# Optimization experiments

Measured on AMD Instinct MI355X. Metric: run time of the kernel, lower is better.

## Reference

```python
import jax, jax.numpy as jnp
import numpy as np
from jax import lax

HEADS = 6      # n_splits // head_ratio
DHEAD = 64     # hidden // n_splits
ALLH = HEADS * DHEAD  # 384
KS = 9         # conv_kernel_size
PAD = (KS - 1) // 2


def setup_inputs() -> dict:
    key = jax.random.key(0)
    ks = jax.random.split(key, 12)
    B, S, H = 8, 1024, 768
    f = jnp.float32
    return {
        "Q": jax.random.normal(ks[0], (B, S, H), f),
        "K": jax.random.normal(ks[1], (B, S, H), f),
        "V": jax.random.normal(ks[2], (B, S, H), f),
        "Wq": jax.random.normal(ks[3], (H, ALLH), f) * 0.02,
        "Wk": jax.random.normal(ks[4], (H, ALLH), f) * 0.02,
        "Wv": jax.random.normal(ks[5], (H, ALLH), f) * 0.02,
        "dw": jax.random.normal(ks[6], (H, KS), f) * 0.02,        # depthwise conv [C,k]
        "pw": jax.random.normal(ks[7], (ALLH, H), f) * 0.02,      # pointwise conv [out,in]
        "sep_bias": jnp.zeros((ALLH,), f),
        "Wck": jax.random.normal(ks[8], (ALLH, HEADS * KS), f) * 0.02,
        "bck": jnp.zeros((HEADS * KS,), f),
        "Wco": jax.random.normal(ks[9], (H, ALLH), f) * 0.02,
        "bco": jnp.zeros((ALLH,), f),
        "gammas": jnp.zeros((HEADS, 1, 1), f),
        "mask": jnp.ones((B, S), jnp.int32),
    }


def _forward(Q, K, V, Wq, Wk, Wv, dw, pw, sep_bias, Wck, bck, Wco, bco, gammas, mask):
    B, S, H = Q.shape
    q = Q @ Wq  # [B,S,ALLH]
    k = K @ Wk
    v = V @ Wv
    # SeparableConv1D on K: depthwise 'same' conv (groups=H) then 1x1 pointwise + bias
    x = K.transpose(0, 2, 1)  # [B,H,S]
    x = lax.conv_general_dilated(x, dw[:, None, :], (1,), [(PAD, PAD)],
                                 dimension_numbers=("NCH", "OIH", "NCH"),
                                 feature_group_count=H)
    keyconv = jnp.einsum("bcs,oc->bso", x, pw) + sep_bias  # [B,S,ALLH]
    # span-dynamic-conv kernel weights, softmax over kernel taps
    conv_attn = keyconv * q
    kern = (conv_attn @ Wck + bck).reshape(B, S, HEADS, KS)
    kern = jax.nn.softmax(kern, axis=-1)
    # unfold V-projection into local windows and apply per-position kernels
    co = V @ Wco + bco                                   # [B,S,ALLH]
    cop = jnp.pad(co, ((0, 0), (PAD, PAD), (0, 0)))
    win = jnp.stack([cop[:, j:j + S, :] for j in range(KS)], axis=-1)  # [B,S,ALLH,KS]
    win = win.reshape(B, S, HEADS, DHEAD, KS)
    conv_out = jnp.einsum("bshdk,bshk->bshd", win, kern)  # [B,S,HEADS,DHEAD]
    # standard attention scores
    q4 = q.reshape(B, S, HEADS, DHEAD).transpose(0, 2, 1, 3)
    k4 = k.reshape(B, S, HEADS, DHEAD).transpose(0, 2, 1, 3)
    v4 = v.reshape(B, S, HEADS, DHEAD).transpose(0, 2, 1, 3)
    scores = jnp.einsum("bhid,bhjd->bhij", q4, k4) / jnp.sqrt(jnp.float32(DHEAD))
    m = (mask != 0)[:, None, None, :]  # key mask [B,1,1,S]
    # monotonic distance scores (no-grad in original -> stop_gradient)
    sc = lax.stop_gradient(scores)
    p_ = jax.nn.softmax(jnp.where(m, sc, -1e32), axis=-1) * m.astype(sc.dtype)
    cum = jnp.cumsum(p_, axis=-1)
    tot = jnp.sum(p_, axis=-1, keepdims=True)
    idx = jnp.arange(S)
    pos = jnp.abs(idx[None, :] - idx[:, None]).astype(jnp.float32)  # |i-j|
    dist = jnp.sqrt(jnp.clip((tot - cum) * pos, 0.0))
    gamma = -jax.nn.softplus(gammas)[None]  # [1,HEADS,1,1]
    effect = jnp.clip(jnp.exp(dist * gamma), 1e-5, 1e5)
    scores2 = jnp.where(m, scores * effect, -1e8)
    probs = jax.nn.softmax(scores2, axis=-1)  # dropout_p=0 -> identity
    ctx = jnp.einsum("bhij,bhjd->bihd", probs, v4)  # [B,S,HEADS,DHEAD]
    out = jnp.concatenate([ctx, conv_out], axis=2).reshape(B, S, 2 * ALLH)
    return out


def reference(Q, K, V, Wq, Wk, Wv, dw, pw, sep_bias, Wck, bck, Wco, bco, gammas, mask):
    return _forward(Q, K, V, Wq, Wk, Wv, dw, pw, sep_bias, Wck, bck, Wco, bco, gammas, mask)
```

## Files before the change

kernel.cpp:

```cpp
#include <hip/hip_runtime.h>
#include <math.h>

#define BATCH 8
#define SEQ   1024
#define HID   768
#define HEADS 6
#define DHEAD 64
#define ALLH  384
#define KS    9
#define PADC  4
#define MROWS (BATCH*SEQ)

typedef __attribute__((ext_vector_type(8))) short bf16x8;
typedef __attribute__((ext_vector_type(4))) short bf16x4;
typedef __attribute__((ext_vector_type(4))) float f32x4;

__device__ __forceinline__ ushort f2bf(float x) {
    unsigned u = __float_as_uint(x);
    unsigned r = (u + 0x7FFFu + ((u >> 16) & 1u)) >> 16;
    return (ushort)r;
}
__device__ __forceinline__ unsigned pk2(float a, float b) {
    return (unsigned)f2bf(a) | ((unsigned)f2bf(b) << 16);
}
__device__ __forceinline__ float fexp2(float x) {
#if __has_builtin(__builtin_amdgcn_exp2f)
    return __builtin_amdgcn_exp2f(x);
#else
    return exp2f(x);
#endif
}
__device__ __forceinline__ float fsqrt(float x) {
#if __has_builtin(__builtin_amdgcn_sqrtf)
    return __builtin_amdgcn_sqrtf(x);
#else
    return __sqrtf(x);
#endif
}
__device__ __forceinline__ unsigned cvtpk(float a, float b) {
    unsigned r; asm("v_cvt_pk_bf16_f32 %0, %1, %2" : "=v"(r) : "v"(a), "v"(b)); return r;
}

__device__ __forceinline__ void mfma16(f32x4& c4, bf16x4 a, bf16x4 b) {
#if __has_builtin(__builtin_amdgcn_mfma_f32_16x16x16bf16_1k)
    c4 = __builtin_amdgcn_mfma_f32_16x16x16bf16_1k(a, b, c4, 0, 0, 0);
#else
    asm volatile("v_mfma_f32_16x16x16_bf16 %0, %1, %2, %0" : "+v"(c4) : "v"(a), "v"(b));
#endif
}

__global__ __launch_bounds__(256) void dconv_kernel(const float* __restrict__ Kin,
                                                    const float* __restrict__ dw,
                                                    ushort* __restrict__ y) {
    const int t = threadIdx.x;
    const int c4l = t & 63;
    const int sg = t >> 6;
    const int c4 = blockIdx.x * 64 + c4l;
    const int s0 = blockIdx.y * 64 + sg * 16;
    const int b = blockIdx.z;
    const int c = c4 * 4;

    const float* base = Kin + (size_t)b * SEQ * HID + c;
    ushort* ybase = y + (size_t)b * SEQ * HID + c;

    float wv[4][KS];
#pragma unroll
    for (int j = 0; j < 4; ++j)
#pragma unroll
        for (int tt = 0; tt < KS; ++tt) wv[j][tt] = dw[(c + j) * KS + tt];

    float4 win[KS];
#pragma unroll
    for (int tt = 0; tt < KS; ++tt) {
        int sj = s0 - PADC + tt;
        win[tt] = (sj >= 0 && sj < SEQ) ? *reinterpret_cast<const float4*>(base + (size_t)sj * HID)
                                        : float4{0.f, 0.f, 0.f, 0.f};
    }

#pragma unroll
    for (int i = 0; i < 16; ++i) {
        const int s = s0 + i;
        float4 acc = {0.f, 0.f, 0.f, 0.f};
#pragma unroll
        for (int tt = 0; tt < KS; ++tt) {
            acc.x += win[tt].x * wv[0][tt];
            acc.y += win[tt].y * wv[1][tt];
            acc.z += win[tt].z * wv[2][tt];
            acc.w += win[tt].w * wv[3][tt];
        }
        uint2 o;
        o.x = pk2(acc.x, acc.y); o.y = pk2(acc.z, acc.w);
        *reinterpret_cast<uint2*>(ybase + (size_t)s * HID) = o;
#pragma unroll
        for (int tt = 0; tt < KS - 1; ++tt) win[tt] = win[tt + 1];
        int sj = s + 1 + PADC;
        win[KS - 1] = (sj < SEQ) ? *reinterpret_cast<const float4*>(base + (size_t)sj * HID)
                                 : float4{0.f, 0.f, 0.f, 0.f};
    }
}

__global__ __launch_bounds__(256) void wcvt_kernel(const float* __restrict__ W0, const float* __restrict__ W1,
                                                   const float* __restrict__ W2, const float* __restrict__ W3,
                                                   ushort* __restrict__ O0, ushort* __restrict__ O1,
                                                   ushort* __restrict__ O2, ushort* __restrict__ O3) {
    __shared__ float t[32][33];
    int wsel = blockIdx.z;
    const float* W = wsel == 0 ? W0 : wsel == 1 ? W1 : wsel == 2 ? W2 : W3;
    ushort* O = wsel == 0 ? O0 : wsel == 1 ? O1 : wsel == 2 ? O2 : O3;
    int kt = blockIdx.x * 32;
    int nt = blockIdx.y * 32;
    int tx = threadIdx.x & 31, ty = threadIdx.x >> 5;
#pragma unroll
    for (int i = 0; i < 4; ++i)
        t[ty + i * 8][tx] = W[(size_t)(kt + ty + i * 8) * ALLH + nt + tx];
    __syncthreads();
#pragma unroll
    for (int i = 0; i < 4; ++i)
        O[(size_t)(nt + ty + i * 8) * HID + kt + tx] = f2bf(t[tx][ty + i * 8]);
}

__global__ __launch_bounds__(256) void pwcvt_kernel(const float* __restrict__ pw, ushort* __restrict__ pwb) {
    int i = blockIdx.x * 256 + threadIdx.x;
    if (i < ALLH * HID) pwb[i] = f2bf(pw[i]);
}

__global__ __launch_bounds__(256) void gemm_all(const float* __restrict__ Q,
                                                const float* __restrict__ Kin,
                                                const float* __restrict__ V,
                                                const ushort* __restrict__ ybf,
                                                const ushort* __restrict__ WqT,
                                                const ushort* __restrict__ WkT,
                                                const ushort* __restrict__ WvT,
                                                const ushort* __restrict__ WcoT,
                                                const ushort* __restrict__ pwT,
                                                const float* __restrict__ bco,
                                                const float* __restrict__ sep_bias,
                                                float* __restrict__ qb,
                                                ushort* __restrict__ qh,
                                                ushort* __restrict__ khm,
                                                ushort* __restrict__ vhm,
                                                float* __restrict__ cob,
                                                float* __restrict__ kcb) {
    __shared__ __align__(16) ushort As[64 * 64];
    __shared__ __align__(16) ushort Bs[64 * 64];

    const int bx = blockIdx.x;
    const int swz = (bx & 7) * 480 + (bx >> 3);
    const int unit = swz / 768;
    const int local = swz % 768;
    const int n0 = (local % 6) * 64;
    const int m0 = (local / 6) * 64;

    const float* Af = unit == 0 ? Q : unit == 1 ? Kin : V;
    const ushort* Ab = ybf;
    const ushort* Bt = unit == 0 ? WqT : unit == 1 ? WkT : unit == 2 ? WvT : unit == 3 ? WcoT : pwT;
    const bool af32 = (unit != 4);

    const int tid = threadIdx.x;
    const int lane = tid & 63;
    const int w = tid >> 6;
    const int g = lane >> 4;
    const int c = lane & 15;

    const int r0 = tid >> 3;
    const int r1 = r0 + 32;
    const int c8 = (tid & 7) * 8;
    const int b0 = r0 * 128 + ((c8 * 2) ^ ((r0 & 7) << 4));
    const int b1 = r1 * 128 + ((c8 * 2) ^ ((r1 & 7) << 4));

    uint4 ar0, ar1, br0, br1;
    float4 f0a, f0b, f1a, f1b;
    auto loadAB = [&](int k0) {
        if (af32) {
            f0a = *reinterpret_cast<const float4*>(&Af[(size_t)(m0 + r0) * HID + k0 + c8]);
            f0b = *reinterpret_cast<const float4*>(&Af[(size_t)(m0 + r0) * HID + k0 + c8 + 4]);
            f1a = *reinterpret_cast<const float4*>(&Af[(size_t)(m0 + r1) * HID + k0 + c8]);
            f1b = *reinterpret_cast<const float4*>(&Af[(size_t)(m0 + r1) * HID + k0 + c8 + 4]);
        } else {
            ar0 = *reinterpret_cast<const uint4*>(&Ab[(size_t)(m0 + r0) * HID + k0 + c8]);
            ar1 = *reinterpret_cast<const uint4*>(&Ab[(size_t)(m0 + r1) * HID + k0 + c8]);
        }
        br0 = *reinterpret_cast<const uint4*>(&Bt[(size_t)(n0 + r0) * HID + k0 + c8]);
        br1 = *reinterpret_cast<const uint4*>(&Bt[(size_t)(n0 + r1) * HID + k0 + c8]);
    };
    loadAB(0);

    f32x4 acc[4] = {{0,0,0,0},{0,0,0,0},{0,0,0,0},{0,0,0,0}};

    const int arow = w * 16 + c;
    const int asw = (arow & 7) << 4;

    for (int ks = 0; ks < 12; ++ks) {
        __syncthreads();
        if (af32) {
            uint4 p0, p1;
            p0.x = pk2(f0a.x, f0a.y); p0.y = pk2(f0a.z, f0a.w);
            p0.z = pk2(f0b.x, f0b.y); p0.w = pk2(f0b.z, f0b.w);
            p1.x = pk2(f1a.x, f1a.y); p1.y = pk2(f1a.z, f1a.w);
            p1.z = pk2(f1b.x, f1b.y); p1.w = pk2(f1b.z, f1b.w);
            *reinterpret_cast<uint4*>((char*)As + b0) = p0;
            *reinterpret_cast<uint4*>((char*)As + b1) = p1;
        } else {
            *reinterpret_cast<uint4*>((char*)As + b0) = ar0;
            *reinterpret_cast<uint4*>((char*)As + b1) = ar1;
        }
        *reinterpret_cast<uint4*>((char*)Bs + b0) = br0;
        *reinterpret_cast<uint4*>((char*)Bs + b1) = br1;
        __syncthreads();
        if (ks < 11) loadAB((ks + 1) * 64);

        bf16x8 af0 = *reinterpret_cast<const bf16x8*>((char*)As + arow * 128 + ((g * 16) ^ asw));
        bf16x8 af1 = *reinterpret_cast<const bf16x8*>((char*)As + arow * 128 + ((64 + g * 16) ^ asw));
#pragma unroll
        for (int nq = 0; nq < 4; ++nq) {
            const int brow = nq * 16 + c;
            const int bsw = (brow & 7) << 4;
            bf16x8 bf0 = *reinterpret_cast<const bf16x8*>((char*)Bs + brow * 128 + ((g * 16) ^ bsw));
            bf16x8 bf1 = *reinterpret_cast<const bf16x8*>((char*)Bs + brow * 128 + ((64 + g * 16) ^ bsw));
            acc[nq] = __builtin_amdgcn_mfma_f32_16x16x32_bf16(af0, bf0, acc[nq], 0, 0, 0);
            acc[nq] = __builtin_amdgcn_mfma_f32_16x16x32_bf16(af1, bf1, acc[nq], 0, 0, 0);
        }
    }

    if (unit == 2) {
        const int head = n0 >> 6;
        const int bb = m0 >> 10;
        const int st = (m0 & 1023) >> 6;
        char* tb = (char*)vhm + (((size_t)(bb * HEADS + head) * 16 + st) * 4096) * 2;
#pragma unroll
        for (int nq = 0; nq < 4; ++nq) {
            const int d = nq * 16 + c;
            unsigned off = (unsigned)d * 128 + (((unsigned)(32 * w + 8 * g)) ^ ((d & 7) << 4));
            uint2 vv;
            vv.x = pk2(acc[nq][0], acc[nq][1]);
            vv.y = pk2(acc[nq][2], acc[nq][3]);
            *reinterpret_cast<uint2*>(tb + off) = vv;
        }
        return;
    }

#pragma unroll
    for (int nq = 0; nq < 4; ++nq) {
        const int n = n0 + nq * 16 + c;
        float bv = 0.f;
        if (unit == 3) bv = bco[n];
        if (unit == 4) bv = sep_bias[n];
#pragma unroll
        for (int r = 0; r < 4; ++r) {
            const int m = m0 + w * 16 + g * 4 + r;
            float v = acc[nq][r] + bv;
            if (unit == 0) {
                qb[(size_t)m * ALLH + n] = v;
                int bb = m >> 10, s = m & 1023;
                int head = n >> 6, d = n & 63;
                qh[(((size_t)bb * HEADS + head) * SEQ + s) * 64 + d] = f2bf(v);
            } else if (unit == 1) {
                int bb = m >> 10, s = m & 1023;
                int head = n >> 6, d = n & 63;
                char* tb = (char*)khm + (((size_t)(bb * HEADS + head) * 16 + (s >> 6)) * 4096) * 2;
                unsigned off = (unsigned)(s & 63) * 128 + (((unsigned)(d * 2)) ^ ((s & 7) << 4));
                *reinterpret_cast<ushort*>(tb + off) = f2bf(v);
            } else if (unit == 3) {
                cob[(size_t)m * ALLH + n] = v;
            } else {
                kcb[(size_t)m * ALLH + n] = v;
            }
        }
    }
}

__global__ __launch_bounds__(256) void spankern_kernel(const float* __restrict__ keyconv,
                                                       const float* __restrict__ q,
                                                       const float* __restrict__ Wck,
                                                       const float* __restrict__ bck,
                                                       float* __restrict__ kern_sm) {
    __shared__ float ca[4][ALLH];
    __shared__ float kv[4][64];
    int row0 = blockIdx.x * 4;
    int tid = threadIdx.x;
    int r = tid >> 6;
    int lane = tid & 63;
    int row = row0 + r;
    for (int e = lane; e < ALLH; e += 64) {
        size_t off = (size_t)row * ALLH + e;
        ca[r][e] = keyconv[off] * q[off];
    }
    __syncthreads();
    float val = 0.f;
    if (lane < HEADS * KS) {
        for (int kidx = 0; kidx < ALLH; ++kidx)
            val += ca[r][kidx] * Wck[kidx * (HEADS * KS) + lane];
        val += bck[lane];
    }
    kv[r][lane] = val;
    __syncthreads();
    if (lane < HEADS) {
        float mx = -INFINITY;
#pragma unroll
        for (int t = 0; t < KS; ++t) mx = fmaxf(mx, kv[r][lane * KS + t]);
        float e[KS];
        float sum = 0.f;
#pragma unroll
        for (int t = 0; t < KS; ++t) {
            e[t] = expf(kv[r][lane * KS + t] - mx);
            sum += e[t];
        }
        float inv = 1.f / sum;
#pragma unroll
        for (int t = 0; t < KS; ++t)
            kern_sm[((size_t)row * HEADS + lane) * KS + t] = e[t] * inv;
    }
}

__global__ __launch_bounds__(256) void convout_kernel(const float* __restrict__ co,
                                                      const float* __restrict__ kern_sm,
                                                      float* __restrict__ out) {
    int idx = blockIdx.x * 256 + threadIdx.x;
    if (idx >= MROWS * (ALLH / 4)) return;
    int c4 = idx % (ALLH / 4);
    int s = (idx / (ALLH / 4)) % SEQ;
    int b = idx / ((ALLH / 4) * SEQ);
    int c = c4 * 4;
    int h = c >> 6;
    const float* ks = &kern_sm[(((size_t)b * SEQ + s) * HEADS + h) * KS];
    float kt[KS];
#pragma unroll
    for (int t = 0; t < KS; ++t) kt[t] = ks[t];
    float4 acc = {0.f, 0.f, 0.f, 0.f};
#pragma unroll
    for (int t = 0; t < KS; ++t) {
        int sj = s + t - PADC;
        if (sj >= 0 && sj < SEQ) {
            const float4 cv = *reinterpret_cast<const float4*>(&co[((size_t)b * SEQ + sj) * ALLH + c]);
            acc.x += cv.x * kt[t];
            acc.y += cv.y * kt[t];
            acc.z += cv.z * kt[t];
            acc.w += cv.w * kt[t];
        }
    }
    *reinterpret_cast<float4*>(&out[((size_t)b * SEQ + s) * (2 * ALLH) + ALLH + c]) = acc;
}

__global__ __launch_bounds__(256) void attn_mfma(const ushort* __restrict__ qh,
                                                 const ushort* __restrict__ kh,
                                                 const ushort* __restrict__ vh,
                                                 const int* __restrict__ mask,
                                                 const float* __restrict__ gammas,
                                                 float* __restrict__ out) {
    __shared__ __align__(16) ushort kbuf[64 * 64];
    __shared__ __align__(16) ushort vbuf[64 * 64];
    __shared__ float s_msk[SEQ];

    const int bid = blockIdx.x;
    const int blk = (bid & 7) * 96 + (bid >> 3);
    const int qt = blk & 15;
    const int h = (blk >> 4) % HEADS;
    const int b = blk / (16 * HEADS);
    const int i0 = qt * 64;
    const int tid = threadIdx.x;
    const int lane = tid & 63;
    const int w = tid >> 6;
    const int g = lane >> 4;
    const int c = lane & 15;

    const float LOG2E = 1.44269504f;
    float g0 = gammas[h];
    float gamma2 = -(fmaxf(g0, 0.f) + log1pf(expf(-fabsf(g0)))) * LOG2E;
    const float SLOG2 = 0.125f * LOG2E;

    const ushort* ktiles = kh + ((size_t)(b * HEADS + h) * 16) * 4096;
    const ushort* vtiles = vh + ((size_t)(b * HEADS + h) * 16) * 4096;
    const ushort* qhb = qh + ((size_t)b * HEADS + h) * SEQ * 64;

    for (int e = tid; e < SEQ; e += 256)
        s_msk[e] = (mask[b * SEQ + e] != 0) ? 1.f : 0.f;

    bf16x8 qf0, qf1;
    {
        const ushort* qrow = qhb + (size_t)(i0 + w * 16 + c) * 64 + g * 8;
        qf0 = *reinterpret_cast<const bf16x8*>(qrow);
        qf1 = *reinterpret_cast<const bf16x8*>(qrow + 32);
    }

    float Tacc = 0.f;
    for (int chk = 0; chk < 16; ++chk) {
        __syncthreads();
        const ushort* ktp = ktiles + chk * 4096;
#pragma unroll
        for (int it = 0; it < 2; ++it) {
            int e16 = (tid + it * 256) * 16;
            *reinterpret_cast<uint4*>((char*)kbuf + e16) =
                *reinterpret_cast<const uint4*>((const char*)ktp + e16);
        }
        __syncthreads();
        const int j0 = chk * 64;
#pragma unroll
        for (int m = 0; m < 4; ++m) {
            f32x4 acc = {0.f, 0.f, 0.f, 0.f};
            int row = m * 16 + c;
            int sw = (row & 7) << 4;
            bf16x8 kf0 = *reinterpret_cast<const bf16x8*>((char*)kbuf + row * 128 + ((g * 16) ^ sw));
            bf16x8 kf1 = *reinterpret_cast<const bf16x8*>((char*)kbuf + row * 128 + ((64 + g * 16) ^ sw));
            acc = __builtin_amdgcn_mfma_f32_16x16x32_bf16(kf0, qf0, acc, 0, 0, 0);
            acc = __builtin_amdgcn_mfma_f32_16x16x32_bf16(kf1, qf1, acc, 0, 0, 0);
#pragma unroll
            for (int r = 0; r < 4; ++r) {
                float mk = s_msk[j0 + m * 16 + g * 4 + r];
                Tacc += mk * fexp2(acc[r] * SLOG2);
            }
        }
    }
    Tacc += __shfl_xor(Tacc, 16, 64);
    Tacc += __shfl_xor(Tacc, 32, 64);
    const float T = Tacc;
    const float invT = (T > 0.f) ? 1.f / T : 0.f;

    f32x4 ctx0 = {0,0,0,0}, ctx1 = {0,0,0,0}, ctx2 = {0,0,0,0}, ctx3 = {0,0,0,0};
    float l2acc = 0.f;
    float base = 0.f;
    const float iq = (float)(i0 + w * 16 + c);
    const unsigned vx = (unsigned)((c & 7) << 4);

    for (int chk = 0; chk < 16; ++chk) {
        __syncthreads();
        const ushort* ktp = ktiles + chk * 4096;
        const ushort* vtp = vtiles + chk * 4096;
#pragma unroll
        for (int it = 0; it < 2; ++it) {
            int e16 = (tid + it * 256) * 16;
            *reinterpret_cast<uint4*>((char*)kbuf + e16) =
                *reinterpret_cast<const uint4*>((const char*)ktp + e16);
            *reinterpret_cast<uint4*>((char*)vbuf + e16) =
                *reinterpret_cast<const uint4*>((const char*)vtp + e16);
        }
        __syncthreads();
        const int j0 = chk * 64;
#pragma unroll
        for (int m = 0; m < 4; ++m) {
            f32x4 acc = {0.f, 0.f, 0.f, 0.f};
            int row = m * 16 + c;
            int sw = (row & 7) << 4;
            bf16x8 kf0 = *reinterpret_cast<const bf16x8*>((char*)kbuf + row * 128 + ((g * 16) ^ sw));
            bf16x8 kf1 = *reinterpret_cast<const bf16x8*>((char*)kbuf + row * 128 + ((64 + g * 16) ^ sw));
            acc = __builtin_amdgcn_mfma_f32_16x16x32_bf16(kf0, qf0, acc, 0, 0, 0);
            acc = __builtin_amdgcn_mfma_f32_16x16x32_bf16(kf1, qf1, acc, 0, 0, 0);

            float sl[4], mk[4], incl[4];
            float li = 0.f;
#pragma unroll
            for (int r = 0; r < 4; ++r) {
                mk[r] = s_msk[j0 + m * 16 + g * 4 + r];
                sl[r] = acc[r] * SLOG2;
                float e = mk[r] * fexp2(sl[r]);
                li += e;
                incl[r] = li;
            }
            float gs = li;
            float up = __shfl_up(gs, 16, 64); if (g >= 1) gs += up;
            up = __shfl_up(gs, 32, 64); if (g >= 2) gs += up;
            float gexcl = gs - li;
            float ttot = __shfl(gs, 48 + c, 64);

            const float dbase = iq - (float)(j0 + m * 16 + g * 4);
            float p2[4];
#pragma unroll
            for (int r = 0; r < 4; ++r) {
                float cum = base + gexcl + incl[r];
                float rem = fmaxf(1.0f - cum * invT, 0.f);
                float pos = fabsf(dbase - (float)r);
                float dist = fsqrt(rem * pos);
                float eff = fmaxf(fexp2(dist * gamma2), 1e-5f);
                p2[r] = mk[r] * fexp2(sl[r] * eff);
                l2acc += p2[r];
            }
            base += ttot;

            union { uint2 u; bf16x4 v; } pu;
            pu.u.x = cvtpk(p2[0], p2[1]);
            pu.u.y = cvtpk(p2[2], p2[3]);
            bf16x4 pa = pu.v;

            const unsigned cb = ((unsigned)(32 * m + 8 * g)) ^ vx;
#pragma unroll
            for (int t = 0; t < 4; ++t) {
                bf16x4 vfrag = *reinterpret_cast<const bf16x4*>((char*)vbuf + (unsigned)(c + 16 * t) * 128 + cb);
                if (t == 0) mfma16(ctx0, pa, vfrag);
                else if (t == 1) mfma16(ctx1, pa, vfrag);
                else if (t == 2) mfma16(ctx2, pa, vfrag);
                else mfma16(ctx3, pa, vfrag);
            }
        }
    }
    l2acc += __shfl_xor(l2acc, 16, 64);
    l2acc += __shfl_xor(l2acc, 32, 64);
    const float invl2 = 1.f / l2acc;

#pragma unroll
    for (int r = 0; r < 4; ++r) {
        float inv_r = __shfl(invl2, g * 4 + r, 64);
        int qrow = i0 + w * 16 + g * 4 + r;
        float* orow = out + ((size_t)b * SEQ + qrow) * (2 * ALLH) + h * DHEAD;
        orow[c +  0] = ctx0[r] * inv_r;
        orow[c + 16] = ctx1[r] * inv_r;
        orow[c + 32] = ctx2[r] * inv_r;
        orow[c + 48] = ctx3[r] * inv_r;
    }
}

extern "C" void kernel_launch(void* const* d_in, const int* in_sizes, int n_in,
                              void* d_out, int out_size, void* d_ws, size_t ws_size,
                              hipStream_t stream) {
    const float* Q = (const float*)d_in[0];
    const float* Kin = (const float*)d_in[1];
    const float* V = (const float*)d_in[2];
    const float* Wq = (const float*)d_in[3];
    const float* Wk = (const float*)d_in[4];
    const float* Wv = (const float*)d_in[5];
    const float* dw = (const float*)d_in[6];
    const float* pw = (const float*)d_in[7];
    const float* sep_bias = (const float*)d_in[8];
    const float* Wck = (const float*)d_in[9];
    const float* bck = (const float*)d_in[10];
    const float* Wco = (const float*)d_in[11];
    const float* bco = (const float*)d_in[12];
    const float* gammas = (const float*)d_in[13];
    const int* mask = (const int*)d_in[14];
    float* out = (float*)d_out;
    float* ws = (float*)d_ws;

    const size_t NP = (size_t)MROWS * ALLH;
    const size_t WSZ = (size_t)ALLH * HID;
    float* qb   = ws;
    float* cob  = qb + NP;
    float* kcb  = cob + NP;
    float* kern = kcb + NP;
    ushort* qh  = (ushort*)(kern + (size_t)MROWS * HEADS * KS);
    ushort* khm = qh + NP;
    ushort* vhm = khm + NP;
    ushort* ybf = vhm + NP;
    ushort* WqT = ybf + (size_t)MROWS * HID;
    ushort* WkT = WqT + WSZ;
    ushort* WvT = WkT + WSZ;
    ushort* WcoT = WvT + WSZ;
    ushort* pwT = WcoT + WSZ;

    dconv_kernel<<<dim3(3, 16, BATCH), 256, 0, stream>>>(Kin, dw, ybf);
    wcvt_kernel<<<dim3(24, 12, 4), 256, 0, stream>>>(Wq, Wk, Wv, Wco, WqT, WkT, WvT, WcoT);
    pwcvt_kernel<<<(ALLH * HID + 255) / 256, 256, 0, stream>>>(pw, pwT);

    gemm_all<<<3840, 256, 0, stream>>>(Q, Kin, V, ybf, WqT, WkT, WvT, WcoT, pwT,
                                       bco, sep_bias, qb, qh, khm, vhm, cob, kcb);

    spankern_kernel<<<MROWS / 4, 256, 0, stream>>>(kcb, qb, Wck, bck, kern);

    convout_kernel<<<(MROWS * (ALLH / 4) + 255) / 256, 256, 0, stream>>>(cob, kern, out);

    attn_mfma<<<BATCH * HEADS * (SEQ / 64), 256, 0, stream>>>(qh, khm, vhm, mask, gammas, out);
}
```

Baseline: 228.9 us.

## Double-buffer GEMM register prefetch, vectorize spankern, slide convout window

The GEMM main loop now holds two register sets (even and odd K-steps) so global loads run two steps ahead and the loop is fully unrolled. The spankern kernel switches to float4 loads for the keyconv*q product and the Wck reduction. The convout kernel is restructured so each thread computes 8 consecutive sequence positions with a sliding 9-tap register window, cutting redundant co loads, and the launch grid is changed to match. The GEMM change raises register pressure, and the convout change launches far fewer threads.

Result: slower. 526.4 us (+130.0%).

```diff
diff --git a/kernel.cpp b/kernel.cpp
--- a/kernel.cpp
+++ b/kernel.cpp
@@ -168,47 +168,44 @@
     const int b0 = r0 * 128 + ((c8 * 2) ^ ((r0 & 7) << 4));
     const int b1 = r1 * 128 + ((c8 * 2) ^ ((r1 & 7) << 4));
 
-    uint4 ar0, ar1, br0, br1;
-    float4 f0a, f0b, f1a, f1b;
-    auto loadAB = [&](int k0) {
+    struct Regs { uint4 ar0, ar1, br0, br1; float4 f0a, f0b, f1a, f1b; };
+    Regs Re, Ro;
+
+    auto loadAB = [&](Regs& R, int k0) {
         if (af32) {
-            f0a = *reinterpret_cast<const float4*>(&Af[(size_t)(m0 + r0) * HID + k0 + c8]);
-            f0b = *reinterpret_cast<const float4*>(&Af[(size_t)(m0 + r0) * HID + k0 + c8 + 4]);
-            f1a = *reinterpret_cast<const float4*>(&Af[(size_t)(m0 + r1) * HID + k0 + c8]);
-            f1b = *reinterpret_cast<const float4*>(&Af[(size_t)(m0 + r1) * HID + k0 + c8 + 4]);
+            R.f0a = *reinterpret_cast<const float4*>(&Af[(size_t)(m0 + r0) * HID + k0 + c8]);
+            R.f0b = *reinterpret_cast<const float4*>(&Af[(size_t)(m0 + r0) * HID + k0 + c8 + 4]);
+            R.f1a = *reinterpret_cast<const float4*>(&Af[(size_t)(m0 + r1) * HID + k0 + c8]);
+            R.f1b = *reinterpret_cast<const float4*>(&Af[(size_t)(m0 + r1) * HID + k0 + c8 + 4]);
         } else {
-            ar0 = *reinterpret_cast<const uint4*>(&Ab[(size_t)(m0 + r0) * HID + k0 + c8]);
-            ar1 = *reinterpret_cast<const uint4*>(&Ab[(size_t)(m0 + r1) * HID + k0 + c8]);
-        }
-        br0 = *reinterpret_cast<const uint4*>(&Bt[(size_t)(n0 + r0) * HID + k0 + c8]);
-        br1 = *reinterpret_cast<const uint4*>(&Bt[(size_t)(n0 + r1) * HID + k0 + c8]);
+            R.ar0 = *reinterpret_cast<const uint4*>(&Ab[(size_t)(m0 + r0) * HID + k0 + c8]);
+            R.ar1 = *reinterpret_cast<const uint4*>(&Ab[(size_t)(m0 + r1) * HID + k0 + c8]);
+        }
+        R.br0 = *reinterpret_cast<const uint4*>(&Bt[(size_t)(n0 + r0) * HID + k0 + c8]);
+        R.br1 = *reinterpret_cast<const uint4*>(&Bt[(size_t)(n0 + r1) * HID + k0 + c8]);
     };
-    loadAB(0);
-
-    f32x4 acc[4] = {{0,0,0,0},{0,0,0,0},{0,0,0,0},{0,0,0,0}};
-
-    const int arow = w * 16 + c;
-    const int asw = (arow & 7) << 4;
-
-    for (int ks = 0; ks < 12; ++ks) {
-        __syncthreads();
+    auto stage = [&](const Regs& R) {
         if (af32) {
             uint4 p0, p1;
-            p0.x = pk2(f0a.x, f0a.y); p0.y = pk2(f0a.z, f0a.w);
-            p0.z = pk2(f0b.x, f0b.y); p0.w = pk2(f0b.z, f0b.w);
-            p1.x = pk2(f1a.x, f1a.y); p1.y = pk2(f1a.z, f1a.w);
-            p1.z = pk2(f1b.x, f1b.y); p1.w = pk2(f1b.z, f1b.w);
+            p0.x = pk2(R.f0a.x, R.f0a.y); p0.y = pk2(R.f0a.z, R.f0a.w);
+            p0.z = pk2(R.f0b.x, R.f0b.y); p0.w = pk2(R.f0b.z, R.f0b.w);
+            p1.x = pk2(R.f1a.x, R.f1a.y); p1.y = pk2(R.f1a.z, R.f1a.w);
+            p1.z = pk2(R.f1b.x, R.f1b.y); p1.w = pk2(R.f1b.z, R.f1b.w);
             *reinterpret_cast<uint4*>((char*)As + b0) = p0;
             *reinterpret_cast<uint4*>((char*)As + b1) = p1;
         } else {
-            *reinterpret_cast<uint4*>((char*)As + b0) = ar0;
-            *reinterpret_cast<uint4*>((char*)As + b1) = ar1;
-        }
-        *reinterpret_cast<uint4*>((char*)Bs + b0) = br0;
-        *reinterpret_cast<uint4*>((char*)Bs + b1) = br1;
-        __syncthreads();
-        if (ks < 11) loadAB((ks + 1) * 64);
-
+            *reinterpret_cast<uint4*>((char*)As + b0) = R.ar0;
+            *reinterpret_cast<uint4*>((char*)As + b1) = R.ar1;
+        }
+        *reinterpret_cast<uint4*>((char*)Bs + b0) = R.br0;
+        *reinterpret_cast<uint4*>((char*)Bs + b1) = R.br1;
+    };
+
+    f32x4 acc[4] = {{0,0,0,0},{0,0,0,0},{0,0,0,0},{0,0,0,0}};
+    const int arow = w * 16 + c;
+    const int asw = (arow & 7) << 4;
+
+    auto compute = [&]() {
         bf16x8 af0 = *reinterpret_cast<const bf16x8*>((char*)As + arow * 128 + ((g * 16) ^ asw));
         bf16x8 af1 = *reinterpret_cast<const bf16x8*>((char*)As + arow * 128 + ((64 + g * 16) ^ asw));
 #pragma unroll
@@ -220,6 +217,22 @@
             acc[nq] = __builtin_amdgcn_mfma_f32_16x16x32_bf16(af0, bf0, acc[nq], 0, 0, 0);
             acc[nq] = __builtin_amdgcn_mfma_f32_16x16x32_bf16(af1, bf1, acc[nq], 0, 0, 0);
         }
+    };
+
+    loadAB(Re, 0);
+    loadAB(Ro, 64);
+#pragma unroll
+    for (int ksp = 0; ksp < 12; ksp += 2) {
+        __syncthreads();
+        stage(Re);
+        __syncthreads();
+        if (ksp + 2 < 12) loadAB(Re, (ksp + 2) * 64);
+        compute();
+        __syncthreads();
+        stage(Ro);
+        __syncthreads();
+        if (ksp + 3 < 12) loadAB(Ro, (ksp + 3) * 64);
+        compute();
     }
 
     if (unit == 2) {
@@ -274,22 +287,31 @@
                                                        const float* __restrict__ Wck,
                                                        const float* __restrict__ bck,
                                                        float* __restrict__ kern_sm) {
-    __shared__ float ca[4][ALLH];
+    __shared__ __align__(16) float ca[4][ALLH];
     __shared__ float kv[4][64];
     int row0 = blockIdx.x * 4;
     int tid = threadIdx.x;
     int r = tid >> 6;
     int lane = tid & 63;
     int row = row0 + r;
-    for (int e = lane; e < ALLH; e += 64) {
-        size_t off = (size_t)row * ALLH + e;
-        ca[r][e] = keyconv[off] * q[off];
+    for (int e = lane; e < ALLH / 4; e += 64) {
+        size_t off = (size_t)row * ALLH + e * 4;
+        const float4 kc = *reinterpret_cast<const float4*>(&keyconv[off]);
+        const float4 qq = *reinterpret_cast<const float4*>(&q[off]);
+        float4 p; p.x = kc.x * qq.x; p.y = kc.y * qq.y; p.z = kc.z * qq.z; p.w = kc.w * qq.w;
+        *reinterpret_cast<float4*>(&ca[r][e * 4]) = p;
     }
     __syncthreads();
     float val = 0.f;
     if (lane < HEADS * KS) {
-        for (int kidx = 0; kidx < ALLH; ++kidx)
-            val += ca[r][kidx] * Wck[kidx * (HEADS * KS) + lane];
+#pragma unroll 4
+        for (int k4 = 0; k4 < ALLH / 4; ++k4) {
+            const float4 cav = *reinterpret_cast<const float4*>(&ca[r][k4 * 4]);
+            val += cav.x * Wck[(k4 * 4 + 0) * (HEADS * KS) + lane];
+            val += cav.y * Wck[(k4 * 4 + 1) * (HEADS * KS) + lane];
+            val += cav.z * Wck[(k4 * 4 + 2) * (HEADS * KS) + lane];
+            val += cav.w * Wck[(k4 * 4 + 3) * (HEADS * KS) + lane];
+        }
         val += bck[lane];
     }
     kv[r][lane] = val;
@@ -315,30 +337,47 @@
 __global__ __launch_bounds__(256) void convout_kernel(const float* __restrict__ co,
                                                       const float* __restrict__ kern_sm,
                                                       float* __restrict__ out) {
-    int idx = blockIdx.x * 256 + threadIdx.x;
-    if (idx >= MROWS * (ALLH / 4)) return;
-    int c4 = idx % (ALLH / 4);
-    int s = (idx / (ALLH / 4)) % SEQ;
-    int b = idx / ((ALLH / 4) * SEQ);
-    int c = c4 * 4;
-    int h = c >> 6;
-    const float* ks = &kern_sm[(((size_t)b * SEQ + s) * HEADS + h) * KS];
-    float kt[KS];
-#pragma unroll
-    for (int t = 0; t < KS; ++t) kt[t] = ks[t];
-    float4 acc = {0.f, 0.f, 0.f, 0.f};
-#pragma unroll
-    for (int t = 0; t < KS; ++t) {
-        int sj = s + t - PADC;
-        if (sj >= 0 && sj < SEQ) {
-            const float4 cv = *reinterpret_cast<const float4*>(&co[((size_t)b * SEQ + sj) * ALLH + c]);
-            acc.x += cv.x * kt[t];
-            acc.y += cv.y * kt[t];
-            acc.z += cv.z * kt[t];
-            acc.w += cv.w * kt[t];
-        }
-    }
-    *reinterpret_cast<float4*>(&out[((size_t)b * SEQ + s) * (2 * ALLH) + ALLH + c]) = acc;
+    const int t = threadIdx.x;
+    const int c4l = t & 31;
+    const int sg = t >> 5;
+    const int c4 = blockIdx.x * 32 + c4l;
+    const int s0 = (blockIdx.y * 8 + sg) * 8;
+    const int b = blockIdx.z;
+    const int c = c4 * 4;
+    const int h = c >> 6;
+
+    const float* base = co + (size_t)b * SEQ * ALLH + c;
+    float* obase = out + (size_t)b * SEQ * (2 * ALLH) + ALLH + c;
+    const float* kbase = kern_sm + ((size_t)b * SEQ) * (HEADS * KS) + h * KS;
+
+    float4 win[KS];
+#pragma unroll
+    for (int tt = 0; tt < KS; ++tt) {
+        int sj = s0 - PADC + tt;
+        win[tt] = (sj >= 0 && sj < SEQ) ? *reinterpret_cast<const float4*>(base + (size_t)sj * ALLH)
+                                        : float4{0.f, 0.f, 0.f, 0.f};
+    }
+
+#pragma unroll
+    for (int i = 0; i < 8; ++i) {
+        const int s = s0 + i;
+        const float* kr = kbase + (size_t)s * (HEADS * KS);
+        float4 acc = {0.f, 0.f, 0.f, 0.f};
+#pragma unroll
+        for (int tt = 0; tt < KS; ++tt) {
+            const float kt = kr[tt];
+            acc.x += win[tt].x * kt;
+            acc.y += win[tt].y * kt;
+            acc.z += win[tt].z * kt;
+            acc.w += win[tt].w * kt;
+        }
+        *reinterpret_cast<float4*>(obase + (size_t)s * (2 * ALLH)) = acc;
+#pragma unroll
+        for (int tt = 0; tt < KS - 1; ++tt) win[tt] = win[tt + 1];
+        int sj = s + 1 + PADC;
+        win[KS - 1] = (sj < SEQ) ? *reinterpret_cast<const float4*>(base + (size_t)sj * ALLH)
+                                 : float4{0.f, 0.f, 0.f, 0.f};
+    }
 }
 
 __global__ __launch_bounds__(256) void attn_mfma(const ushort* __restrict__ qh,
@@ -553,7 +592,7 @@
 
     spankern_kernel<<<MROWS / 4, 256, 0, stream>>>(kcb, qb, Wck, bck, kern);
 
-    convout_kernel<<<(MROWS * (ALLH / 4) + 255) / 256, 256, 0, stream>>>(cob, kern, out);
+    convout_kernel<<<dim3(3, 16, BATCH), 256, 0, stream>>>(cob, kern, out);
 
     attn_mfma<<<BATCH * HEADS * (SEQ / 64), 256, 0, stream>>>(qh, khm, vhm, mask, gammas, out);
 }
```
